# Optimization experiments

Hardware: AMD Instinct MI355X
Metric: run time of the kernel (lower is better)

Reference implementation:

```python
import jax, jax.numpy as jnp
import numpy as np

HEAD_NUM = 7
HEAD_DIM = 64
HIDDEN = 896

def rotate_half(t):
    d = t.shape[-1] // 2
    return jnp.concatenate([-t[..., d:], t[..., :d]], axis=-1)

def setup_inputs() -> dict:
    key = jax.random.key(0)
    ks = jax.random.split(key, 11)
    B, S = 4, 2048
    proj = HEAD_NUM * HEAD_DIM  # 448
    sc_in = 1.0 / np.sqrt(HIDDEN)
    sc_pr = 1.0 / np.sqrt(proj)
    pos = jnp.arange(S)[:, None].astype(jnp.float32)
    inv_freq = 1.0 / (10000.0 ** (jnp.arange(0, HEAD_DIM, 2, dtype=jnp.float32) / HEAD_DIM))
    ang = pos * inv_freq[None, :]              # [S, D/2]
    emb = jnp.concatenate([ang, ang], axis=-1) # [S, D]
    return {
        'x': jax.random.normal(ks[0], (B, S, HIDDEN), jnp.float32),
        'cos': jnp.cos(emb),
        'sin': jnp.sin(emb),
        'q_w': jax.random.normal(ks[1], (proj, HIDDEN), jnp.float32) * sc_in,
        'q_b': jax.random.normal(ks[2], (proj,), jnp.float32) * 0.01,
        'k_w': jax.random.normal(ks[3], (proj, HIDDEN), jnp.float32) * sc_in,
        'k_b': jax.random.normal(ks[4], (proj,), jnp.float32) * 0.01,
        'v_w': jax.random.normal(ks[5], (proj, HIDDEN), jnp.float32) * sc_in,
        'v_b': jax.random.normal(ks[6], (proj,), jnp.float32) * 0.01,
        'o_w': jax.random.normal(ks[7], (HIDDEN, proj), jnp.float32) * sc_pr,
        'o_b': jax.random.normal(ks[8], (HIDDEN,), jnp.float32) * 0.01,
    }

def reference(x, cos, sin, q_w, q_b, k_w, k_b, v_w, v_b, o_w, o_b):
    B, S, _ = x.shape
    def proj(w, b):
        y = jnp.einsum('bsh,ph->bsp', x, w) + b          # [B,S,H*D]
        return y.reshape(B, S, HEAD_NUM, HEAD_DIM).transpose(0, 2, 1, 3)  # [B,H,S,D]
    q = proj(q_w, q_b)
    k = proj(k_w, k_b)
    v = proj(v_w, v_b)
    c = cos[None, None, :, :]
    s = sin[None, None, :, :]
    q = q * c + rotate_half(q) * s
    k = k * c + rotate_half(k) * s
    scores = jnp.einsum('bhqd,bhkd->bhqk', q, k) / np.sqrt(HEAD_DIM)
    attn = jax.nn.softmax(scores, axis=-1)
    out = jnp.einsum('bhqk,bhkd->bhqd', attn, v)          # [B,H,S,D]
    out = out.transpose(0, 2, 1, 3).reshape(B, S, HEAD_NUM * HEAD_DIM)
    return jnp.einsum('bsp,hp->bsh', out, o_w) + o_b
```

## Files before the change

### kernel.cpp

```cpp
#include <hip/hip_runtime.h>

typedef _Float16 f16;
typedef __attribute__((ext_vector_type(8))) _Float16 f16x8;
typedef __attribute__((ext_vector_type(4))) _Float16 f16x4;
typedef __attribute__((ext_vector_type(4))) float f32x4;

#define MFMA(a,b,c) __builtin_amdgcn_mfma_f32_16x16x32_f16(a,b,c,0,0,0)

constexpr int HN = 7, HD = 64, HID = 896, PR = 448;
constexpr int NB = 4, NS = 2048, NM = NB * NS;
constexpr float LOG2E = 1.44269504088896f;

__device__ __forceinline__ void gload16(const f16* g, f16* l) {
    __builtin_amdgcn_global_load_lds(
        (const __attribute__((address_space(1))) void*)g,
        (__attribute__((address_space(3))) void*)l,
        16, 0, 0);
}

__device__ __forceinline__ int xcd_swz(int orig, int per) {
    return (orig & 7) * per + (orig >> 3);
}

__global__ __launch_bounds__(256) void conv_kernel(
    const float* __restrict__ x,  const float* __restrict__ qw,
    const float* __restrict__ kw, const float* __restrict__ vw,
    const float* __restrict__ ow,
    f16* __restrict__ xb, f16* __restrict__ wq, f16* __restrict__ wk,
    f16* __restrict__ wv, f16* __restrict__ wo)
{
    const int XV = NM * HID / 4;
    const int WV = PR * HID / 4;
    const int TOT = XV + 4 * WV;
    int64_t stride = (int64_t)gridDim.x * blockDim.x;
    for (int64_t v = (int64_t)blockIdx.x * 256 + threadIdx.x; v < TOT; v += stride) {
        const float* src; f16* dst; int64_t off;
        if (v < XV)               { src = x;  dst = xb; off = v; }
        else if (v < XV + WV)     { src = qw; dst = wq; off = v - XV; }
        else if (v < XV + 2*WV)   { src = kw; dst = wk; off = v - XV - WV; }
        else if (v < XV + 3*WV)   { src = vw; dst = wv; off = v - XV - 2*WV; }
        else                      { src = ow; dst = wo; off = v - XV - 3*WV; }
        f32x4 fv = *((const f32x4*)src + off);
        f16x4 hv = { (f16)fv[0], (f16)fv[1], (f16)fv[2], (f16)fv[3] };
        *((f16x4*)dst + off) = hv;
    }
}

__global__ __launch_bounds__(256) void qkv_gemm(
    const f16* __restrict__ xb, const f16* __restrict__ wq,
    const f16* __restrict__ wk, const f16* __restrict__ wv,
    const float* __restrict__ qb, const float* __restrict__ kb,
    const float* __restrict__ vb,
    const float* __restrict__ cosT, const float* __restrict__ sinT,
    f16* __restrict__ Q, f16* __restrict__ K, f16* __restrict__ Vt)
{
    extern __shared__ char smem[];
    f16* As = (f16*)smem;
    f16* Bs = (f16*)(smem + 128*64*2);
    f16* Cs = (f16*)smem;

    const int wg = xcd_swz(blockIdx.x, 168);
    const int tynt = wg % 21, mt = wg / 21;
    const int ty = tynt / 7, nt = tynt % 7;
    const int m0 = mt * 128, n0 = nt * 64;

    const f16* w = (ty == 0) ? wq : (ty == 1) ? wk : wv;
    const float* bias = (ty == 0) ? qb : (ty == 1) ? kb : vb;

    const int tid = threadIdx.x;
    const int wv_ = tid >> 6, lane = tid & 63;
    const int wm = wv_ >> 1, wn = wv_ & 1;
    const int g = lane >> 4, lr = lane & 15;
    const int lrow = lane >> 3;
    const int cswz = (lane & 7) ^ (lrow & 7);

    const int ch0 = (g ^ (lr & 7)) * 8;
    const int ch1 = ((4 + g) ^ (lr & 7)) * 8;

    f32x4 acc[4][2] = {};

    for (int k0 = 0; k0 < HID; k0 += 64) {
        #pragma unroll
        for (int p = 0; p < 4; p++) {
            int rt = wv_*32 + p*8;
            gload16(xb + (int64_t)(m0 + rt + lrow)*HID + k0 + cswz*8, As + rt*64);
        }
        #pragma unroll
        for (int p = 0; p < 2; p++) {
            int rt = wv_*16 + p*8;
            gload16(w + (int64_t)(n0 + rt + lrow)*HID + k0 + cswz*8, Bs + rt*64);
        }
        __syncthreads();
        #pragma unroll
        for (int kc = 0; kc < 2; kc++) {
            const int ch = kc ? ch1 : ch0;
            f16x8 af[4], bf[2];
            #pragma unroll
            for (int fm = 0; fm < 4; fm++)
                af[fm] = *(const f16x8*)(As + (wm*64 + fm*16 + lr)*64 + ch);
            #pragma unroll
            for (int fn = 0; fn < 2; fn++)
                bf[fn] = *(const f16x8*)(Bs + (wn*32 + fn*16 + lr)*64 + ch);
            #pragma unroll
            for (int fm = 0; fm < 4; fm++)
                #pragma unroll
                for (int fn = 0; fn < 2; fn++)
                    acc[fm][fn] = MFMA(af[fm], bf[fn], acc[fm][fn]);
        }
        __syncthreads();
    }

    float bias_f[2];
    #pragma unroll
    for (int fn = 0; fn < 2; fn++) bias_f[fn] = bias[n0 + wn*32 + fn*16 + lr];
    #pragma unroll
    for (int fm = 0; fm < 4; fm++)
        #pragma unroll
        for (int fn = 0; fn < 2; fn++)
            #pragma unroll
            for (int j = 0; j < 4; j++)
                Cs[(wm*64 + fm*16 + g*4 + j)*72 + wn*32 + fn*16 + lr] = (f16)(acc[fm][fn][j] + bias_f[fn]);
    __syncthreads();

    const int b = m0 / NS;
    const int s0 = m0 % NS;
    const int64_t bhbase = ((int64_t)(b*HN + nt)) * NS * HD;

    if (ty < 2) {
        const float scale = (ty == 0) ? 0.125f * LOG2E : 1.0f;
        const int r = tid >> 1, d0 = (tid & 1) * 32, s = s0 + r;
        const f16* crow = Cs + r*72;
        f16 vals[32];
        if (d0 == 0) {
            #pragma unroll
            for (int i = 0; i < 8; i++) {
                f32x4 cl = *(const f32x4*)(cosT + s*64 + i*4);
                f32x4 sl = *(const f32x4*)(sinT + s*64 + i*4);
                #pragma unroll
                for (int j = 0; j < 4; j++) {
                    float lo = (float)crow[i*4+j], hi = (float)crow[32 + i*4+j];
                    vals[i*4 + j] = (f16)((lo*cl[j] - hi*sl[j]) * scale);
                }
            }
        } else {
            #pragma unroll
            for (int i = 0; i < 8; i++) {
                f32x4 cl = *(const f32x4*)(cosT + s*64 + 32 + i*4);
                f32x4 sl = *(const f32x4*)(sinT + s*64 + 32 + i*4);
                #pragma unroll
                for (int j = 0; j < 4; j++) {
                    float lo = (float)crow[i*4+j], hi = (float)crow[32 + i*4+j];
                    vals[i*4 + j] = (f16)((hi*cl[j] + lo*sl[j]) * scale);
                }
            }
        }
        if (ty == 0) {
            f16* p = Q + bhbase + (int64_t)s * HD + d0;
            #pragma unroll
            for (int i = 0; i < 4; i++)
                *(f16x8*)(p + i*8) = *(f16x8*)(vals + i*8);
        } else {
            int tt = (s0 >> 6) + (r >> 6);
            int rt = r & 63;
            f16* base = K + bhbase + tt*4096 + rt*64;
            #pragma unroll
            for (int i = 0; i < 4; i++)
                *(f16x8*)(base + (((d0>>3) + i) ^ (rt & 7))*8) = *(f16x8*)(vals + i*8);
        }
    } else {
        const int d = tid & 63, sblk = tid >> 6, si0 = sblk * 32;
        f16 vals[32];
        #pragma unroll
        for (int i = 0; i < 32; i++)
            vals[i] = Cs[(si0 + i)*72 + d];
        int tt = (s0 >> 6) + (si0 >> 6);
        int sb = si0 & 63;
        f16* base = Vt + bhbase + tt*4096 + d*64;
        #pragma unroll
        for (int i = 0; i < 4; i++)
            *(f16x8*)(base + (((sb>>3) + i) ^ (d & 7))*8) = *(f16x8*)(vals + i*8);
    }
}

__global__ __launch_bounds__(256) void attn_kernel(
    const f16* __restrict__ Q, const f16* __restrict__ K2,
    const f16* __restrict__ V2, f16* __restrict__ O)
{
    __shared__ __align__(16) f16 KVs[2][2][4096];
    __shared__ __align__(16) f16 Pl[4][32][64];

    const int wg = xcd_swz(blockIdx.x, 56);
    const int qb = wg & 15, bh = wg >> 4;
    const int tid = threadIdx.x, w = tid >> 6, lane = tid & 63;
    const int g = lane >> 4, lr = lane & 15;
    const int q0 = qb * 128 + w * 32;

    const int64_t bhoff = (int64_t)bh * NS * HD;
    const f16* Qp = Q + bhoff;
    const f16* Kp = K2 + bhoff;
    const f16* Vp = V2 + bhoff;

    f16x8 aq[2][2];
    #pragma unroll
    for (int qh = 0; qh < 2; qh++) {
        aq[qh][0] = *(const f16x8*)(Qp + (q0 + qh*16 + lr) * HD + g * 8);
        aq[qh][1] = *(const f16x8*)(Qp + (q0 + qh*16 + lr) * HD + 32 + g * 8);
    }

    const int stoff = w * 1024 + lane * 8;
    const int ldoff = w * 1024;

    gload16(Kp + stoff,       &KVs[0][0][ldoff]);
    gload16(Kp + stoff + 512, &KVs[0][0][ldoff + 512]);
    gload16(Vp + stoff,       &KVs[0][1][ldoff]);
    gload16(Vp + stoff + 512, &KVs[0][1][ldoff + 512]);
    __syncthreads();

    f32x4 accO[2][4] = {};
    float mrun[2] = {-1e30f, -1e30f}, srun[2] = {0.f, 0.f};

    const int ch0 = (g ^ (lr & 7)) * 8;
    const int ch1 = ((4 + g) ^ (lr & 7)) * 8;
    const int pswz = (lr & 7) * 8;

    int buf = 0;
    for (int t = 0; t < NS / 64; ++t) {
        if (t + 1 < NS / 64) {
            const f16* ks = Kp + (t + 1) * 4096 + stoff;
            const f16* vs = Vp + (t + 1) * 4096 + stoff;
            gload16(ks,       &KVs[buf ^ 1][0][ldoff]);
            gload16(ks + 512, &KVs[buf ^ 1][0][ldoff + 512]);
            gload16(vs,       &KVs[buf ^ 1][1][ldoff]);
            gload16(vs + 512, &KVs[buf ^ 1][1][ldoff + 512]);
        }
        const f16* Ks = &KVs[buf][0][0];
        const f16* Vs = &KVs[buf][1][0];

        f32x4 sf[2][4];
        __builtin_amdgcn_s_setprio(1);
        #pragma unroll
        for (int kt = 0; kt < 4; ++kt) {
            const f16* kl = Ks + (kt * 16 + lr) * 64;
            f16x8 k0 = *(const f16x8*)(kl + ch0);
            f16x8 k1 = *(const f16x8*)(kl + ch1);
            #pragma unroll
            for (int qh = 0; qh < 2; ++qh) {
                f32x4 z = {};
                z = MFMA(k0, aq[qh][0], z);
                z = MFMA(k1, aq[qh][1], z);
                sf[qh][kt] = z;
            }
        }
        __builtin_amdgcn_s_setprio(0);

        float pmax[2];
        #pragma unroll
        for (int qh = 0; qh < 2; ++qh) {
            float m0a = fmaxf(fmaxf(sf[qh][0][0], sf[qh][0][1]), fmaxf(sf[qh][0][2], sf[qh][0][3]));
            float m1a = fmaxf(fmaxf(sf[qh][1][0], sf[qh][1][1]), fmaxf(sf[qh][1][2], sf[qh][1][3]));
            float m2a = fmaxf(fmaxf(sf[qh][2][0], sf[qh][2][1]), fmaxf(sf[qh][2][2], sf[qh][2][3]));
            float m3a = fmaxf(fmaxf(sf[qh][3][0], sf[qh][3][1]), fmaxf(sf[qh][3][2], sf[qh][3][3]));
            float pm = fmaxf(fmaxf(m0a, m1a), fmaxf(m2a, m3a));
            pm = fmaxf(pm, __shfl_xor(pm, 16, 64));
            pm = fmaxf(pm, __shfl_xor(pm, 32, 64));
            pmax[qh] = pm;
        }

        if (!__all(pmax[0] - mrun[0] <= 8.0f && pmax[1] - mrun[1] <= 8.0f)) {
            #pragma unroll
            for (int qh = 0; qh < 2; ++qh) {
                float mn = fmaxf(mrun[qh], pmax[qh]);
                float corr = exp2f(mrun[qh] - mn);
                mrun[qh] = mn;
                srun[qh] *= corr;
                #pragma unroll
                for (int fn = 0; fn < 4; ++fn)
                    #pragma unroll
                    for (int j = 0; j < 4; ++j)
                        accO[qh][fn][j] *= corr;
            }
        }

        #pragma unroll
        for (int qh = 0; qh < 2; ++qh) {
            #pragma unroll
            for (int kt = 0; kt < 4; ++kt)
                #pragma unroll
                for (int j = 0; j < 4; ++j)
                    sf[qh][kt][j] = exp2f(sf[qh][kt][j] - mrun[qh]);
            float s0a = (sf[qh][0][0] + sf[qh][0][1]) + (sf[qh][0][2] + sf[qh][0][3]);
            float s1a = (sf[qh][1][0] + sf[qh][1][1]) + (sf[qh][1][2] + sf[qh][1][3]);
            float s2a = (sf[qh][2][0] + sf[qh][2][1]) + (sf[qh][2][2] + sf[qh][2][3]);
            float s3a = (sf[qh][3][0] + sf[qh][3][1]) + (sf[qh][3][2] + sf[qh][3][3]);
            float tsum = (s0a + s1a) + (s2a + s3a);
            tsum += __shfl_xor(tsum, 16, 64);
            tsum += __shfl_xor(tsum, 32, 64);
            srun[qh] += tsum;
            #pragma unroll
            for (int kt = 0; kt < 4; ++kt) {
                f16x4 pk = { (f16)sf[qh][kt][0], (f16)sf[qh][kt][1],
                             (f16)sf[qh][kt][2], (f16)sf[qh][kt][3] };
                *(f16x4*)&Pl[w][qh*16 + lr][(kt*16 + g*4) ^ pswz] = pk;
            }
        }

        f16x8 p0[2], p1[2];
        #pragma unroll
        for (int qh = 0; qh < 2; ++qh) {
            p0[qh] = *(const f16x8*)&Pl[w][qh*16 + lr][ch0];
            p1[qh] = *(const f16x8*)&Pl[w][qh*16 + lr][ch1];
        }

        __builtin_amdgcn_s_setprio(1);
        #pragma unroll
        for (int fn = 0; fn < 4; ++fn) {
            const f16* vl = Vs + (fn * 16 + lr) * 64;
            f16x8 v0 = *(const f16x8*)(vl + ch0);
            f16x8 v1 = *(const f16x8*)(vl + ch1);
            #pragma unroll
            for (int qh = 0; qh < 2; ++qh) {
                accO[qh][fn] = MFMA(v0, p0[qh], accO[qh][fn]);
                accO[qh][fn] = MFMA(v1, p1[qh], accO[qh][fn]);
            }
        }
        __builtin_amdgcn_s_setprio(0);
        __syncthreads();
        buf ^= 1;
    }

    const int b = bh / HN, h = bh % HN;
    #pragma unroll
    for (int qh = 0; qh < 2; ++qh) {
        const float inv = 1.0f / srun[qh];
        const int q = q0 + qh*16 + lr;
        f16* orow = O + ((int64_t)b * NS + q) * PR + h * HD;
        #pragma unroll
        for (int fn = 0; fn < 4; ++fn) {
            f16x4 hv = { (f16)(accO[qh][fn][0] * inv), (f16)(accO[qh][fn][1] * inv),
                         (f16)(accO[qh][fn][2] * inv), (f16)(accO[qh][fn][3] * inv) };
            *(f16x4*)(orow + fn * 16 + g * 4) = hv;
        }
    }
}

__global__ __launch_bounds__(256) void oproj_gemm(
    const f16* __restrict__ Ob, const f16* __restrict__ wo,
    const float* __restrict__ ob, float* __restrict__ out)
{
    extern __shared__ char smem[];
    f16* As = (f16*)smem;
    f16* Bs = (f16*)(smem + 128*64*2);

    const int wg = xcd_swz(blockIdx.x, 112);
    const int nt = wg % 14, mt = wg / 14;
    const int m0 = mt*128, n0 = nt*64;
    const int tid = threadIdx.x;
    const int wv_ = tid >> 6, lane = tid & 63;
    const int wm = wv_ >> 1, wn = wv_ & 1;
    const int g = lane >> 4, lr = lane & 15;
    const int lrow = lane >> 3;
    const int cswz = (lane & 7) ^ (lrow & 7);

    const int ch0 = (g ^ (lr & 7)) * 8;
    const int ch1 = ((4 + g) ^ (lr & 7)) * 8;

    f32x4 acc[4][2] = {};

    for (int k0 = 0; k0 < PR; k0 += 64) {
        #pragma unroll
        for (int p = 0; p < 4; p++) {
            int rt = wv_*32 + p*8;
            gload16(Ob + (int64_t)(m0 + rt + lrow)*PR + k0 + cswz*8, As + rt*64);
        }
        #pragma unroll
        for (int p = 0; p < 2; p++) {
            int rt = wv_*16 + p*8;
            gload16(wo + (int64_t)(n0 + rt + lrow)*PR + k0 + cswz*8, Bs + rt*64);
        }
        __syncthreads();
        #pragma unroll
        for (int kc = 0; kc < 2; kc++) {
            const int ch = kc ? ch1 : ch0;
            f16x8 af[4], bf[2];
            #pragma unroll
            for (int fm = 0; fm < 4; fm++)
                af[fm] = *(const f16x8*)(As + (wm*64 + fm*16 + lr)*64 + ch);
            #pragma unroll
            for (int fn = 0; fn < 2; fn++)
                bf[fn] = *(const f16x8*)(Bs + (wn*32 + fn*16 + lr)*64 + ch);
            #pragma unroll
            for (int fm = 0; fm < 4; fm++)
                #pragma unroll
                for (int fn = 0; fn < 2; fn++)
                    acc[fm][fn] = MFMA(af[fm], bf[fn], acc[fm][fn]);
        }
        __syncthreads();
    }

    float bias_f[2];
    #pragma unroll
    for (int fn = 0; fn < 2; fn++) bias_f[fn] = ob[n0 + wn*32 + fn*16 + lr];
    #pragma unroll
    for (int fm = 0; fm < 4; fm++)
        #pragma unroll
        for (int fn = 0; fn < 2; fn++)
            #pragma unroll
            for (int j = 0; j < 4; j++) {
                int row = m0 + wm*64 + fm*16 + g*4 + j;
                int col = n0 + wn*32 + fn*16 + lr;
                out[(int64_t)row*HID + col] = acc[fm][fn][j] + bias_f[fn];
            }
}

extern "C" void kernel_launch(void* const* d_in, const int* in_sizes, int n_in,
                              void* d_out, int out_size, void* d_ws, size_t ws_size,
                              hipStream_t stream) {
    const float* x    = (const float*)d_in[0];
    const float* cosT = (const float*)d_in[1];
    const float* sinT = (const float*)d_in[2];
    const float* qw   = (const float*)d_in[3];
    const float* qb   = (const float*)d_in[4];
    const float* kw   = (const float*)d_in[5];
    const float* kb   = (const float*)d_in[6];
    const float* vw   = (const float*)d_in[7];
    const float* vb   = (const float*)d_in[8];
    const float* ow   = (const float*)d_in[9];
    const float* ob   = (const float*)d_in[10];
    float* out = (float*)d_out;

    char* ws = (char*)d_ws;
    f16* xb = (f16*)ws;  ws += (size_t)NM * HID * 2;
    f16* wqf = (f16*)ws; ws += (size_t)PR * HID * 2;
    f16* wkf = (f16*)ws; ws += (size_t)PR * HID * 2;
    f16* wvf = (f16*)ws; ws += (size_t)PR * HID * 2;
    f16* wof = (f16*)ws; ws += (size_t)HID * PR * 2;
    f16* Qb = (f16*)ws;  ws += (size_t)NB * HN * NS * HD * 2;
    f16* Kb = (f16*)ws;  ws += (size_t)NB * HN * NS * HD * 2;
    f16* Vt = (f16*)ws;  ws += (size_t)NB * HN * HD * NS * 2;
    f16* Obuf = (f16*)ws; ws += (size_t)NM * PR * 2;

    conv_kernel<<<dim3(2048), dim3(256), 0, stream>>>(x, qw, kw, vw, ow, xb, wqf, wkf, wvf, wof);
    qkv_gemm<<<dim3(1344), dim3(256), 24576, stream>>>(xb, wqf, wkf, wvf, qb, kb, vb, cosT, sinT, Qb, Kb, Vt);
    attn_kernel<<<dim3(448), dim3(256), 0, stream>>>(Qb, Kb, Vt, Obuf);
    oproj_gemm<<<dim3(896), dim3(256), 24576, stream>>>(Obuf, wof, ob, out);
}
```

Before: 222.6 us.

## Fuse QKV projections per tile, compute softmax row sum via MFMA, widen oproj tiles

Result: slower. 241.6 us (+8.5%).

```diff
diff --git a/kernel.cpp b/kernel.cpp
--- a/kernel.cpp
+++ b/kernel.cpp
@@ -46,7 +46,7 @@
     }
 }
 
-__global__ __launch_bounds__(256) void qkv_gemm(
+__global__ __launch_bounds__(256) void qkv_fused(
     const f16* __restrict__ xb, const f16* __restrict__ wq,
     const f16* __restrict__ wk, const f16* __restrict__ wv,
     const float* __restrict__ qb, const float* __restrict__ kb,
@@ -59,13 +59,10 @@
     f16* Bs = (f16*)(smem + 128*64*2);
     f16* Cs = (f16*)smem;
 
-    const int wg = xcd_swz(blockIdx.x, 168);
-    const int tynt = wg % 21, mt = wg / 21;
-    const int ty = tynt / 7, nt = tynt % 7;
+    const int wg = xcd_swz(blockIdx.x, 56);
+    const int mt = wg / 7, nt = wg % 7;
     const int m0 = mt * 128, n0 = nt * 64;
-
-    const f16* w = (ty == 0) ? wq : (ty == 1) ? wk : wv;
-    const float* bias = (ty == 0) ? qb : (ty == 1) ? kb : vb;
+    const f16* wts[3] = { wq, wk, wv };
 
     const int tid = threadIdx.x;
     const int wv_ = tid >> 6, lane = tid & 63;
@@ -77,7 +74,7 @@
     const int ch0 = (g ^ (lr & 7)) * 8;
     const int ch1 = ((4 + g) ^ (lr & 7)) * 8;
 
-    f32x4 acc[4][2] = {};
+    f32x4 acc[3][4][2] = {};
 
     for (int k0 = 0; k0 < HID; k0 += 64) {
         #pragma unroll
@@ -86,99 +83,112 @@
             gload16(xb + (int64_t)(m0 + rt + lrow)*HID + k0 + cswz*8, As + rt*64);
         }
         #pragma unroll
-        for (int p = 0; p < 2; p++) {
-            int rt = wv_*16 + p*8;
-            gload16(w + (int64_t)(n0 + rt + lrow)*HID + k0 + cswz*8, Bs + rt*64);
-        }
+        for (int ty = 0; ty < 3; ty++)
+            #pragma unroll
+            for (int p = 0; p < 2; p++) {
+                int rt = wv_*16 + p*8;
+                gload16(wts[ty] + (int64_t)(n0 + rt + lrow)*HID + k0 + cswz*8,
+                        Bs + ty*4096 + rt*64);
+            }
         __syncthreads();
         #pragma unroll
         for (int kc = 0; kc < 2; kc++) {
             const int ch = kc ? ch1 : ch0;
-            f16x8 af[4], bf[2];
+            f16x8 af[4];
             #pragma unroll
             for (int fm = 0; fm < 4; fm++)
                 af[fm] = *(const f16x8*)(As + (wm*64 + fm*16 + lr)*64 + ch);
             #pragma unroll
-            for (int fn = 0; fn < 2; fn++)
-                bf[fn] = *(const f16x8*)(Bs + (wn*32 + fn*16 + lr)*64 + ch);
-            #pragma unroll
-            for (int fm = 0; fm < 4; fm++)
+            for (int ty = 0; ty < 3; ty++) {
+                f16x8 bf[2];
                 #pragma unroll
                 for (int fn = 0; fn < 2; fn++)
-                    acc[fm][fn] = MFMA(af[fm], bf[fn], acc[fm][fn]);
-        }
-        __syncthreads();
-    }
-
-    float bias_f[2];
-    #pragma unroll
-    for (int fn = 0; fn < 2; fn++) bias_f[fn] = bias[n0 + wn*32 + fn*16 + lr];
-    #pragma unroll
-    for (int fm = 0; fm < 4; fm++)
-        #pragma unroll
-        for (int fn = 0; fn < 2; fn++)
-            #pragma unroll
-            for (int j = 0; j < 4; j++)
-                Cs[(wm*64 + fm*16 + g*4 + j)*72 + wn*32 + fn*16 + lr] = (f16)(acc[fm][fn][j] + bias_f[fn]);
-    __syncthreads();
+                    bf[fn] = *(const f16x8*)(Bs + ty*4096 + (wn*32 + fn*16 + lr)*64 + ch);
+                #pragma unroll
+                for (int fm = 0; fm < 4; fm++)
+                    #pragma unroll
+                    for (int fn = 0; fn < 2; fn++)
+                        acc[ty][fm][fn] = MFMA(af[fm], bf[fn], acc[ty][fm][fn]);
+            }
+        }
+        __syncthreads();
+    }
 
     const int b = m0 / NS;
     const int s0 = m0 % NS;
     const int64_t bhbase = ((int64_t)(b*HN + nt)) * NS * HD;
 
-    if (ty < 2) {
-        const float scale = (ty == 0) ? 0.125f * LOG2E : 1.0f;
-        const int r = tid >> 1, d0 = (tid & 1) * 32, s = s0 + r;
-        const f16* crow = Cs + r*72;
-        f16 vals[32];
-        if (d0 == 0) {
-            #pragma unroll
-            for (int i = 0; i < 8; i++) {
-                f32x4 cl = *(const f32x4*)(cosT + s*64 + i*4);
-                f32x4 sl = *(const f32x4*)(sinT + s*64 + i*4);
-                #pragma unroll
-                for (int j = 0; j < 4; j++) {
-                    float lo = (float)crow[i*4+j], hi = (float)crow[32 + i*4+j];
-                    vals[i*4 + j] = (f16)((lo*cl[j] - hi*sl[j]) * scale);
+    #pragma unroll
+    for (int ty = 0; ty < 3; ty++) {
+        const float* bias = (ty == 0) ? qb : (ty == 1) ? kb : vb;
+        float bias_f[2];
+        #pragma unroll
+        for (int fn = 0; fn < 2; fn++) bias_f[fn] = bias[n0 + wn*32 + fn*16 + lr];
+        #pragma unroll
+        for (int fm = 0; fm < 4; fm++)
+            #pragma unroll
+            for (int fn = 0; fn < 2; fn++)
+                #pragma unroll
+                for (int j = 0; j < 4; j++)
+                    Cs[(wm*64 + fm*16 + g*4 + j)*72 + wn*32 + fn*16 + lr] =
+                        (f16)(acc[ty][fm][fn][j] + bias_f[fn]);
+        __syncthreads();
+
+        if (ty < 2) {
+            const float scale = (ty == 0) ? 0.125f * LOG2E : 1.0f;
+            const int r = tid >> 1, d0 = (tid & 1) * 32, s = s0 + r;
+            const f16* crow = Cs + r*72;
+            f16 vals[32];
+            if (d0 == 0) {
+                #pragma unroll
+                for (int i = 0; i < 8; i++) {
+                    f32x4 cl = *(const f32x4*)(cosT + s*64 + i*4);
+                    f32x4 sl = *(const f32x4*)(sinT + s*64 + i*4);
+                    #pragma unroll
+                    for (int j = 0; j < 4; j++) {
+                        float lo = (float)crow[i*4+j], hi = (float)crow[32 + i*4+j];
+                        vals[i*4 + j] = (f16)((lo*cl[j] - hi*sl[j]) * scale);
+                    }
                 }
+            } else {
+                #pragma unroll
+                for (int i = 0; i < 8; i++) {
+                    f32x4 cl = *(const f32x4*)(cosT + s*64 + 32 + i*4);
+                    f32x4 sl = *(const f32x4*)(sinT + s*64 + 32 + i*4);
+                    #pragma unroll
+                    for (int j = 0; j < 4; j++) {
+                        float lo = (float)crow[i*4+j], hi = (float)crow[32 + i*4+j];
+                        vals[i*4 + j] = (f16)((hi*cl[j] + lo*sl[j]) * scale);
+                    }
+                }
+            }
+            if (ty == 0) {
+                f16* p = Q + bhbase + (int64_t)s * HD + d0;
+                #pragma unroll
+                for (int i = 0; i < 4; i++)
+                    *(f16x8*)(p + i*8) = *(f16x8*)(vals + i*8);
+            } else {
+                int tt = (s0 >> 6) + (r >> 6);
+                int rt = r & 63;
+                f16* base = K + bhbase + tt*4096 + rt*64;
+                #pragma unroll
+                for (int i = 0; i < 4; i++)
+                    *(f16x8*)(base + (((d0>>3) + i) ^ (rt & 7))*8) = *(f16x8*)(vals + i*8);
             }
         } else {
-            #pragma unroll
-            for (int i = 0; i < 8; i++) {
-                f32x4 cl = *(const f32x4*)(cosT + s*64 + 32 + i*4);
-                f32x4 sl = *(const f32x4*)(sinT + s*64 + 32 + i*4);
-                #pragma unroll
-                for (int j = 0; j < 4; j++) {
-                    float lo = (float)crow[i*4+j], hi = (float)crow[32 + i*4+j];
-                    vals[i*4 + j] = (f16)((hi*cl[j] + lo*sl[j]) * scale);
-                }
-            }
-        }
-        if (ty == 0) {
-            f16* p = Q + bhbase + (int64_t)s * HD + d0;
+            const int d = tid & 63, sblk = tid >> 6, si0 = sblk * 32;
+            f16 vals[32];
+            #pragma unroll
+            for (int i = 0; i < 32; i++)
+                vals[i] = Cs[(si0 + i)*72 + d];
+            int tt = (s0 >> 6) + (si0 >> 6);
+            int sb = si0 & 63;
+            f16* base = Vt + bhbase + tt*4096 + d*64;
             #pragma unroll
             for (int i = 0; i < 4; i++)
-                *(f16x8*)(p + i*8) = *(f16x8*)(vals + i*8);
-        } else {
-            int tt = (s0 >> 6) + (r >> 6);
-            int rt = r & 63;
-            f16* base = K + bhbase + tt*4096 + rt*64;
-            #pragma unroll
-            for (int i = 0; i < 4; i++)
-                *(f16x8*)(base + (((d0>>3) + i) ^ (rt & 7))*8) = *(f16x8*)(vals + i*8);
-        }
-    } else {
-        const int d = tid & 63, sblk = tid >> 6, si0 = sblk * 32;
-        f16 vals[32];
-        #pragma unroll
-        for (int i = 0; i < 32; i++)
-            vals[i] = Cs[(si0 + i)*72 + d];
-        int tt = (s0 >> 6) + (si0 >> 6);
-        int sb = si0 & 63;
-        f16* base = Vt + bhbase + tt*4096 + d*64;
-        #pragma unroll
-        for (int i = 0; i < 4; i++)
-            *(f16x8*)(base + (((sb>>3) + i) ^ (d & 7))*8) = *(f16x8*)(vals + i*8);
+                *(f16x8*)(base + (((sb>>3) + i) ^ (d & 7))*8) = *(f16x8*)(vals + i*8);
+        }
+        __syncthreads();
     }
 }
 
@@ -206,6 +216,8 @@
         aq[qh][0] = *(const f16x8*)(Qp + (q0 + qh*16 + lr) * HD + g * 8);
         aq[qh][1] = *(const f16x8*)(Qp + (q0 + qh*16 + lr) * HD + 32 + g * 8);
     }
+    const f16x8 vONE = { (f16)1.f, (f16)1.f, (f16)1.f, (f16)1.f,
+                         (f16)1.f, (f16)1.f, (f16)1.f, (f16)1.f };
 
     const int stoff = w * 1024 + lane * 8;
     const int ldoff = w * 1024;
@@ -216,8 +228,8 @@
     gload16(Vp + stoff + 512, &KVs[0][1][ldoff + 512]);
     __syncthreads();
 
-    f32x4 accO[2][4] = {};
-    float mrun[2] = {-1e30f, -1e30f}, srun[2] = {0.f, 0.f};
+    f32x4 accO[2][5] = {};
+    float mrun[2] = {-1e30f, -1e30f};
 
     const int ch0 = (g ^ (lr & 7)) * 8;
     const int ch1 = ((4 + g) ^ (lr & 7)) * 8;
@@ -272,9 +284,8 @@
                 float mn = fmaxf(mrun[qh], pmax[qh]);
                 float corr = exp2f(mrun[qh] - mn);
                 mrun[qh] = mn;
-                srun[qh] *= corr;
-                #pragma unroll
-                for (int fn = 0; fn < 4; ++fn)
+                #pragma unroll
+                for (int fn = 0; fn < 5; ++fn)
                     #pragma unroll
                     for (int j = 0; j < 4; ++j)
                         accO[qh][fn][j] *= corr;
@@ -288,14 +299,6 @@
                 #pragma unroll
                 for (int j = 0; j < 4; ++j)
                     sf[qh][kt][j] = exp2f(sf[qh][kt][j] - mrun[qh]);
-            float s0a = (sf[qh][0][0] + sf[qh][0][1]) + (sf[qh][0][2] + sf[qh][0][3]);
-            float s1a = (sf[qh][1][0] + sf[qh][1][1]) + (sf[qh][1][2] + sf[qh][1][3]);
-            float s2a = (sf[qh][2][0] + sf[qh][2][1]) + (sf[qh][2][2] + sf[qh][2][3]);
-            float s3a = (sf[qh][3][0] + sf[qh][3][1]) + (sf[qh][3][2] + sf[qh][3][3]);
-            float tsum = (s0a + s1a) + (s2a + s3a);
-            tsum += __shfl_xor(tsum, 16, 64);
-            tsum += __shfl_xor(tsum, 32, 64);
-            srun[qh] += tsum;
             #pragma unroll
             for (int kt = 0; kt < 4; ++kt) {
                 f16x4 pk = { (f16)sf[qh][kt][0], (f16)sf[qh][kt][1],
@@ -323,6 +326,11 @@
                 accO[qh][fn] = MFMA(v1, p1[qh], accO[qh][fn]);
             }
         }
+        #pragma unroll
+        for (int qh = 0; qh < 2; ++qh) {
+            accO[qh][4] = MFMA(vONE, p0[qh], accO[qh][4]);
+            accO[qh][4] = MFMA(vONE, p1[qh], accO[qh][4]);
+        }
         __builtin_amdgcn_s_setprio(0);
         __syncthreads();
         buf ^= 1;
@@ -331,7 +339,7 @@
     const int b = bh / HN, h = bh % HN;
     #pragma unroll
     for (int qh = 0; qh < 2; ++qh) {
-        const float inv = 1.0f / srun[qh];
+        const float inv = 1.0f / accO[qh][4][0];
         const int q = q0 + qh*16 + lr;
         f16* orow = O + ((int64_t)b * NS + q) * PR + h * HD;
         #pragma unroll
@@ -351,9 +359,9 @@
     f16* As = (f16*)smem;
     f16* Bs = (f16*)(smem + 128*64*2);
 
-    const int wg = xcd_swz(blockIdx.x, 112);
-    const int nt = wg % 14, mt = wg / 14;
-    const int m0 = mt*128, n0 = nt*64;
+    const int wg = xcd_swz(blockIdx.x, 56);
+    const int nt = wg % 7, mt = wg / 7;
+    const int m0 = mt*128, n0 = nt*128;
     const int tid = threadIdx.x;
     const int wv_ = tid >> 6, lane = tid & 63;
     const int wm = wv_ >> 1, wn = wv_ & 1;
@@ -364,7 +372,7 @@
     const int ch0 = (g ^ (lr & 7)) * 8;
     const int ch1 = ((4 + g) ^ (lr & 7)) * 8;
 
-    f32x4 acc[4][2] = {};
+    f32x4 acc[4][4] = {};
 
     for (int k0 = 0; k0 < PR; k0 += 64) {
         #pragma unroll
@@ -373,41 +381,41 @@
             gload16(Ob + (int64_t)(m0 + rt + lrow)*PR + k0 + cswz*8, As + rt*64);
         }
         #pragma unroll
-        for (int p = 0; p < 2; p++) {
-            int rt = wv_*16 + p*8;
+        for (int p = 0; p < 4; p++) {
+            int rt = wv_*32 + p*8;
             gload16(wo + (int64_t)(n0 + rt + lrow)*PR + k0 + cswz*8, Bs + rt*64);
         }
         __syncthreads();
         #pragma unroll
         for (int kc = 0; kc < 2; kc++) {
             const int ch = kc ? ch1 : ch0;
-            f16x8 af[4], bf[2];
+            f16x8 af[4], bf[4];
             #pragma unroll
             for (int fm = 0; fm < 4; fm++)
                 af[fm] = *(const f16x8*)(As + (wm*64 + fm*16 + lr)*64 + ch);
             #pragma unroll
-            for (int fn = 0; fn < 2; fn++)
-                bf[fn] = *(const f16x8*)(Bs + (wn*32 + fn*16 + lr)*64 + ch);
+            for (int fn = 0; fn < 4; fn++)
+                bf[fn] = *(const f16x8*)(Bs + (wn*64 + fn*16 + lr)*64 + ch);
             #pragma unroll
             for (int fm = 0; fm < 4; fm++)
                 #pragma unroll
-                for (int fn = 0; fn < 2; fn++)
+                for (int fn = 0; fn < 4; fn++)
                     acc[fm][fn] = MFMA(af[fm], bf[fn], acc[fm][fn]);
         }
         __syncthreads();
     }
 
-    float bias_f[2];
+    float bias_f[4];
     #pragma unroll
-    for (int fn = 0; fn < 2; fn++) bias_f[fn] = ob[n0 + wn*32 + fn*16 + lr];
+    for (int fn = 0; fn < 4; fn++) bias_f[fn] = ob[n0 + wn*64 + fn*16 + lr];
     #pragma unroll
     for (int fm = 0; fm < 4; fm++)
         #pragma unroll
-        for (int fn = 0; fn < 2; fn++)
+        for (int fn = 0; fn < 4; fn++)
             #pragma unroll
             for (int j = 0; j < 4; j++) {
                 int row = m0 + wm*64 + fm*16 + g*4 + j;
-                int col = n0 + wn*32 + fn*16 + lr;
+                int col = n0 + wn*64 + fn*16 + lr;
                 out[(int64_t)row*HID + col] = acc[fm][fn][j] + bias_f[fn];
             }
 }
@@ -440,7 +448,7 @@
     f16* Obuf = (f16*)ws; ws += (size_t)NM * PR * 2;
 
     conv_kernel<<<dim3(2048), dim3(256), 0, stream>>>(x, qw, kw, vw, ow, xb, wqf, wkf, wvf, wof);
-    qkv_gemm<<<dim3(1344), dim3(256), 24576, stream>>>(xb, wqf, wkf, wvf, qb, kb, vb, cosT, sinT, Qb, Kb, Vt);
+    qkv_fused<<<dim3(448), dim3(256), 40960, stream>>>(xb, wqf, wkf, wvf, qb, kb, vb, cosT, sinT, Qb, Kb, Vt);
     attn_kernel<<<dim3(448), dim3(256), 0, stream>>>(Qb, Kb, Vt, Obuf);
-    oproj_gemm<<<dim3(896), dim3(256), 24576, stream>>>(Obuf, wof, ob, out);
-}
+    oproj_gemm<<<dim3(448), dim3(256), 32768, stream>>>(Obuf, wof, ob, out);
+}
```

## Double-buffer GEMM tiles, halve attention block size, compute row sums via MFMA

Applied to the files above, without the earlier changes.

After: 226.8 us. Within noise of the previous version (+1.9%).

```diff
diff --git a/kernel.cpp b/kernel.cpp
--- a/kernel.cpp
+++ b/kernel.cpp
@@ -56,7 +56,7 @@
 {
     extern __shared__ char smem[];
     f16* As = (f16*)smem;
-    f16* Bs = (f16*)(smem + 128*64*2);
+    f16* Bs = (f16*)(smem + 2*128*64*2);
     f16* Cs = (f16*)smem;
 
     const int wg = xcd_swz(blockIdx.x, 168);
@@ -78,37 +78,58 @@
     const int ch1 = ((4 + g) ^ (lr & 7)) * 8;
 
     f32x4 acc[4][2] = {};
-
-    for (int k0 = 0; k0 < HID; k0 += 64) {
-        #pragma unroll
-        for (int p = 0; p < 4; p++) {
-            int rt = wv_*32 + p*8;
-            gload16(xb + (int64_t)(m0 + rt + lrow)*HID + k0 + cswz*8, As + rt*64);
-        }
-        #pragma unroll
-        for (int p = 0; p < 2; p++) {
-            int rt = wv_*16 + p*8;
-            gload16(w + (int64_t)(n0 + rt + lrow)*HID + k0 + cswz*8, Bs + rt*64);
-        }
+    constexpr int NT = HID / 64;
+
+    #pragma unroll
+    for (int p = 0; p < 4; p++) {
+        int rt = wv_*32 + p*8;
+        gload16(xb + (int64_t)(m0 + rt + lrow)*HID + cswz*8, As + rt*64);
+    }
+    #pragma unroll
+    for (int p = 0; p < 2; p++) {
+        int rt = wv_*16 + p*8;
+        gload16(w + (int64_t)(n0 + rt + lrow)*HID + cswz*8, Bs + rt*64);
+    }
+
+    int cur = 0;
+    for (int kt = 0; kt < NT; ++kt) {
         __syncthreads();
+        if (kt + 1 < NT) {
+            const int k0 = (kt + 1) * 64;
+            #pragma unroll
+            for (int p = 0; p < 4; p++) {
+                int rt = wv_*32 + p*8;
+                gload16(xb + (int64_t)(m0 + rt + lrow)*HID + k0 + cswz*8,
+                        As + (cur^1)*8192 + rt*64);
+            }
+            #pragma unroll
+            for (int p = 0; p < 2; p++) {
+                int rt = wv_*16 + p*8;
+                gload16(w + (int64_t)(n0 + rt + lrow)*HID + k0 + cswz*8,
+                        Bs + (cur^1)*4096 + rt*64);
+            }
+        }
+        const f16* Ac = As + cur*8192;
+        const f16* Bc = Bs + cur*4096;
         #pragma unroll
         for (int kc = 0; kc < 2; kc++) {
             const int ch = kc ? ch1 : ch0;
             f16x8 af[4], bf[2];
             #pragma unroll
             for (int fm = 0; fm < 4; fm++)
-                af[fm] = *(const f16x8*)(As + (wm*64 + fm*16 + lr)*64 + ch);
+                af[fm] = *(const f16x8*)(Ac + (wm*64 + fm*16 + lr)*64 + ch);
             #pragma unroll
             for (int fn = 0; fn < 2; fn++)
-                bf[fn] = *(const f16x8*)(Bs + (wn*32 + fn*16 + lr)*64 + ch);
+                bf[fn] = *(const f16x8*)(Bc + (wn*32 + fn*16 + lr)*64 + ch);
             #pragma unroll
             for (int fm = 0; fm < 4; fm++)
                 #pragma unroll
                 for (int fn = 0; fn < 2; fn++)
                     acc[fm][fn] = MFMA(af[fm], bf[fn], acc[fm][fn]);
         }
-        __syncthreads();
-    }
+        cur ^= 1;
+    }
+    __syncthreads();
 
     float bias_f[2];
     #pragma unroll
@@ -182,18 +203,18 @@
     }
 }
 
-__global__ __launch_bounds__(256) void attn_kernel(
+__global__ __launch_bounds__(128) void attn_kernel(
     const f16* __restrict__ Q, const f16* __restrict__ K2,
     const f16* __restrict__ V2, f16* __restrict__ O)
 {
     __shared__ __align__(16) f16 KVs[2][2][4096];
-    __shared__ __align__(16) f16 Pl[4][32][64];
-
-    const int wg = xcd_swz(blockIdx.x, 56);
-    const int qb = wg & 15, bh = wg >> 4;
+    __shared__ __align__(16) f16 Pl[2][32][64];
+
+    const int wg = xcd_swz(blockIdx.x, 112);
+    const int qb = wg & 31, bh = wg >> 5;
     const int tid = threadIdx.x, w = tid >> 6, lane = tid & 63;
     const int g = lane >> 4, lr = lane & 15;
-    const int q0 = qb * 128 + w * 32;
+    const int q0 = qb * 64 + w * 32;
 
     const int64_t bhoff = (int64_t)bh * NS * HD;
     const f16* Qp = Q + bhoff;
@@ -206,18 +227,21 @@
         aq[qh][0] = *(const f16x8*)(Qp + (q0 + qh*16 + lr) * HD + g * 8);
         aq[qh][1] = *(const f16x8*)(Qp + (q0 + qh*16 + lr) * HD + 32 + g * 8);
     }
-
-    const int stoff = w * 1024 + lane * 8;
-    const int ldoff = w * 1024;
-
-    gload16(Kp + stoff,       &KVs[0][0][ldoff]);
-    gload16(Kp + stoff + 512, &KVs[0][0][ldoff + 512]);
-    gload16(Vp + stoff,       &KVs[0][1][ldoff]);
-    gload16(Vp + stoff + 512, &KVs[0][1][ldoff + 512]);
+    const f16x8 vONE = { (f16)1.f, (f16)1.f, (f16)1.f, (f16)1.f,
+                         (f16)1.f, (f16)1.f, (f16)1.f, (f16)1.f };
+
+    const int stoff = w * 2048 + lane * 8;
+    const int ldoff = w * 2048;
+
+    #pragma unroll
+    for (int o = 0; o < 4; o++) {
+        gload16(Kp + stoff + o*512, &KVs[0][0][ldoff + o*512]);
+        gload16(Vp + stoff + o*512, &KVs[0][1][ldoff + o*512]);
+    }
     __syncthreads();
 
-    f32x4 accO[2][4] = {};
-    float mrun[2] = {-1e30f, -1e30f}, srun[2] = {0.f, 0.f};
+    f32x4 accO[2][5] = {};
+    float mrun[2] = {-1e30f, -1e30f};
 
     const int ch0 = (g ^ (lr & 7)) * 8;
     const int ch1 = ((4 + g) ^ (lr & 7)) * 8;
@@ -228,10 +252,11 @@
         if (t + 1 < NS / 64) {
             const f16* ks = Kp + (t + 1) * 4096 + stoff;
             const f16* vs = Vp + (t + 1) * 4096 + stoff;
-            gload16(ks,       &KVs[buf ^ 1][0][ldoff]);
-            gload16(ks + 512, &KVs[buf ^ 1][0][ldoff + 512]);
-            gload16(vs,       &KVs[buf ^ 1][1][ldoff]);
-            gload16(vs + 512, &KVs[buf ^ 1][1][ldoff + 512]);
+            #pragma unroll
+            for (int o = 0; o < 4; o++) {
+                gload16(ks + o*512, &KVs[buf ^ 1][0][ldoff + o*512]);
+                gload16(vs + o*512, &KVs[buf ^ 1][1][ldoff + o*512]);
+            }
         }
         const f16* Ks = &KVs[buf][0][0];
         const f16* Vs = &KVs[buf][1][0];
@@ -272,9 +297,8 @@
                 float mn = fmaxf(mrun[qh], pmax[qh]);
                 float corr = exp2f(mrun[qh] - mn);
                 mrun[qh] = mn;
-                srun[qh] *= corr;
-                #pragma unroll
-                for (int fn = 0; fn < 4; ++fn)
+                #pragma unroll
+                for (int fn = 0; fn < 5; ++fn)
                     #pragma unroll
                     for (int j = 0; j < 4; ++j)
                         accO[qh][fn][j] *= corr;
@@ -288,14 +312,6 @@
                 #pragma unroll
                 for (int j = 0; j < 4; ++j)
                     sf[qh][kt][j] = exp2f(sf[qh][kt][j] - mrun[qh]);
-            float s0a = (sf[qh][0][0] + sf[qh][0][1]) + (sf[qh][0][2] + sf[qh][0][3]);
-            float s1a = (sf[qh][1][0] + sf[qh][1][1]) + (sf[qh][1][2] + sf[qh][1][3]);
-            float s2a = (sf[qh][2][0] + sf[qh][2][1]) + (sf[qh][2][2] + sf[qh][2][3]);
-            float s3a = (sf[qh][3][0] + sf[qh][3][1]) + (sf[qh][3][2] + sf[qh][3][3]);
-            float tsum = (s0a + s1a) + (s2a + s3a);
-            tsum += __shfl_xor(tsum, 16, 64);
-            tsum += __shfl_xor(tsum, 32, 64);
-            srun[qh] += tsum;
             #pragma unroll
             for (int kt = 0; kt < 4; ++kt) {
                 f16x4 pk = { (f16)sf[qh][kt][0], (f16)sf[qh][kt][1],
@@ -323,6 +339,11 @@
                 accO[qh][fn] = MFMA(v1, p1[qh], accO[qh][fn]);
             }
         }
+        #pragma unroll
+        for (int qh = 0; qh < 2; ++qh) {
+            accO[qh][4] = MFMA(vONE, p0[qh], accO[qh][4]);
+            accO[qh][4] = MFMA(vONE, p1[qh], accO[qh][4]);
+        }
         __builtin_amdgcn_s_setprio(0);
         __syncthreads();
         buf ^= 1;
@@ -331,7 +352,7 @@
     const int b = bh / HN, h = bh % HN;
     #pragma unroll
     for (int qh = 0; qh < 2; ++qh) {
-        const float inv = 1.0f / srun[qh];
+        const float inv = 1.0f / accO[qh][4][0];
         const int q = q0 + qh*16 + lr;
         f16* orow = O + ((int64_t)b * NS + q) * PR + h * HD;
         #pragma unroll
@@ -349,7 +370,7 @@
 {
     extern __shared__ char smem[];
     f16* As = (f16*)smem;
-    f16* Bs = (f16*)(smem + 128*64*2);
+    f16* Bs = (f16*)(smem + 2*128*64*2);
 
     const int wg = xcd_swz(blockIdx.x, 112);
     const int nt = wg % 14, mt = wg / 14;
@@ -365,36 +386,56 @@
     const int ch1 = ((4 + g) ^ (lr & 7)) * 8;
 
     f32x4 acc[4][2] = {};
-
-    for (int k0 = 0; k0 < PR; k0 += 64) {
-        #pragma unroll
-        for (int p = 0; p < 4; p++) {
-            int rt = wv_*32 + p*8;
-            gload16(Ob + (int64_t)(m0 + rt + lrow)*PR + k0 + cswz*8, As + rt*64);
-        }
-        #pragma unroll
-        for (int p = 0; p < 2; p++) {
-            int rt = wv_*16 + p*8;
-            gload16(wo + (int64_t)(n0 + rt + lrow)*PR + k0 + cswz*8, Bs + rt*64);
-        }
+    constexpr int NT = PR / 64;
+
+    #pragma unroll
+    for (int p = 0; p < 4; p++) {
+        int rt = wv_*32 + p*8;
+        gload16(Ob + (int64_t)(m0 + rt + lrow)*PR + cswz*8, As + rt*64);
+    }
+    #pragma unroll
+    for (int p = 0; p < 2; p++) {
+        int rt = wv_*16 + p*8;
+        gload16(wo + (int64_t)(n0 + rt + lrow)*PR + cswz*8, Bs + rt*64);
+    }
+
+    int cur = 0;
+    for (int kt = 0; kt < NT; ++kt) {
         __syncthreads();
+        if (kt + 1 < NT) {
+            const int k0 = (kt + 1) * 64;
+            #pragma unroll
+            for (int p = 0; p < 4; p++) {
+                int rt = wv_*32 + p*8;
+                gload16(Ob + (int64_t)(m0 + rt + lrow)*PR + k0 + cswz*8,
+                        As + (cur^1)*8192 + rt*64);
+            }
+            #pragma unroll
+            for (int p = 0; p < 2; p++) {
+                int rt = wv_*16 + p*8;
+                gload16(wo + (int64_t)(n0 + rt + lrow)*PR + k0 + cswz*8,
+                        Bs + (cur^1)*4096 + rt*64);
+            }
+        }
+        const f16* Ac = As + cur*8192;
+        const f16* Bc = Bs + cur*4096;
         #pragma unroll
         for (int kc = 0; kc < 2; kc++) {
             const int ch = kc ? ch1 : ch0;
             f16x8 af[4], bf[2];
             #pragma unroll
             for (int fm = 0; fm < 4; fm++)
-                af[fm] = *(const f16x8*)(As + (wm*64 + fm*16 + lr)*64 + ch);
+                af[fm] = *(const f16x8*)(Ac + (wm*64 + fm*16 + lr)*64 + ch);
             #pragma unroll
             for (int fn = 0; fn < 2; fn++)
-                bf[fn] = *(const f16x8*)(Bs + (wn*32 + fn*16 + lr)*64 + ch);
+                bf[fn] = *(const f16x8*)(Bc + (wn*32 + fn*16 + lr)*64 + ch);
             #pragma unroll
             for (int fm = 0; fm < 4; fm++)
                 #pragma unroll
                 for (int fn = 0; fn < 2; fn++)
                     acc[fm][fn] = MFMA(af[fm], bf[fn], acc[fm][fn]);
         }
-        __syncthreads();
+        cur ^= 1;
     }
 
     float bias_f[2];
@@ -440,7 +481,7 @@
     f16* Obuf = (f16*)ws; ws += (size_t)NM * PR * 2;
 
     conv_kernel<<<dim3(2048), dim3(256), 0, stream>>>(x, qw, kw, vw, ow, xb, wqf, wkf, wvf, wof);
-    qkv_gemm<<<dim3(1344), dim3(256), 24576, stream>>>(xb, wqf, wkf, wvf, qb, kb, vb, cosT, sinT, Qb, Kb, Vt);
-    attn_kernel<<<dim3(448), dim3(256), 0, stream>>>(Qb, Kb, Vt, Obuf);
-    oproj_gemm<<<dim3(896), dim3(256), 24576, stream>>>(Obuf, wof, ob, out);
-}
+    qkv_gemm<<<dim3(1344), dim3(256), 49152, stream>>>(xb, wqf, wkf, wvf, qb, kb, vb, cosT, sinT, Qb, Kb, Vt);
+    attn_kernel<<<dim3(896), dim3(128), 0, stream>>>(Qb, Kb, Vt, Obuf);
+    oproj_gemm<<<dim3(896), dim3(256), 49152, stream>>>(Obuf, wof, ob, out);
+}
```
